# Kernel tuning notes

Hardware: AMD Instinct MI355X
Metric: run time of the kernel (lower is better)

Reference implementation:

```python
import jax, jax.numpy as jnp
import numpy as np

N = 50000   # nodes
E = 800000  # edges
H = 4       # heads
C = 64      # per-head channels (= hidden_channels, concat=False)
IN = 64     # in_channels
OUT = 32    # out_channels
EPS = 1e-5


def setup_inputs() -> dict:
    key = jax.random.key(0)
    ks = jax.random.split(key, 16)

    def lin(k, i, o):
        return (jax.random.normal(k, (i, o), jnp.float32) / np.sqrt(i)).astype(jnp.float32)

    inp = {}
    inp["x"] = jax.random.normal(ks[0], (N, IN), jnp.float32)
    inp["edge_index"] = jax.random.randint(ks[1], (2, E), 0, N, dtype=jnp.int32)
    # conv1 (in=IN)
    inp["Wq1"] = lin(ks[2], IN, H * C); inp["bq1"] = jnp.zeros((H * C,), jnp.float32)
    inp["Wk1"] = lin(ks[3], IN, H * C); inp["bk1"] = jnp.zeros((H * C,), jnp.float32)
    inp["Wv1"] = lin(ks[4], IN, H * C); inp["bv1"] = jnp.zeros((H * C,), jnp.float32)
    inp["Ws1"] = lin(ks[5], IN, C);     inp["bs1"] = jnp.zeros((C,), jnp.float32)
    # conv2 (in=head_out=C)
    inp["Wq2"] = lin(ks[6], C, H * C); inp["bq2"] = jnp.zeros((H * C,), jnp.float32)
    inp["Wk2"] = lin(ks[7], C, H * C); inp["bk2"] = jnp.zeros((H * C,), jnp.float32)
    inp["Wv2"] = lin(ks[8], C, H * C); inp["bv2"] = jnp.zeros((H * C,), jnp.float32)
    inp["Ws2"] = lin(ks[9], C, C);     inp["bs2"] = jnp.zeros((C,), jnp.float32)
    # shared LayerNorm over head_out=C, final Linear C->OUT
    inp["ln_g"] = jnp.ones((C,), jnp.float32)
    inp["ln_b"] = jnp.zeros((C,), jnp.float32)
    inp["Wf"] = lin(ks[10], C, OUT)
    inp["bf"] = jnp.zeros((OUT,), jnp.float32)
    return inp


def _layernorm(x, g, b):
    mu = jnp.mean(x, axis=-1, keepdims=True)
    var = jnp.mean(jnp.square(x - mu), axis=-1, keepdims=True)
    return (x - mu) * jax.lax.rsqrt(var + EPS) * g + b


def _transformer_conv(x, src, dst, Wq, bq, Wk, bk, Wv, bv, Ws, bs):
    # PyG TransformerConv, concat=False, beta=False, root_weight=True, eval dropout
    n = x.shape[0]
    q = (x @ Wq + bq).reshape(n, H, C)
    k = (x @ Wk + bk).reshape(n, H, C)
    v = (x @ Wv + bv).reshape(n, H, C)
    # per-edge attention logits [E, H]
    alpha = jnp.einsum('ehc,ehc->eh', q[dst], k[src]) / np.sqrt(C)
    # segment softmax over incoming edges of each dst node
    amax = jax.ops.segment_max(alpha, dst, num_segments=n)            # [N, H]
    ex = jnp.exp(alpha - amax[dst])                                   # [E, H]
    denom = jax.ops.segment_sum(ex, dst, num_segments=n)              # [N, H]
    attn = ex / (denom[dst] + 1e-16)                                  # [E, H]
    msg = attn[:, :, None] * v[src]                                   # [E, H, C]
    out = jax.ops.segment_sum(msg, dst, num_segments=n)               # [N, H, C]
    out = out.mean(axis=1)                                            # concat=False -> head mean
    return out + x @ Ws + bs                                          # skip connection


def reference(x, edge_index, Wq1, bq1, Wk1, bk1, Wv1, bv1, Ws1, bs1,
              Wq2, bq2, Wk2, bk2, Wv2, bv2, Ws2, bs2, ln_g, ln_b, Wf, bf):
    src, dst = edge_index[0], edge_index[1]
    h = _transformer_conv(x, src, dst, Wq1, bq1, Wk1, bk1, Wv1, bv1, Ws1, bs1)
    h = jax.nn.relu(_layernorm(h, ln_g, ln_b))  # dropout = identity (eval)
    h = _transformer_conv(h, src, dst, Wq2, bq2, Wk2, bk2, Wv2, bv2, Ws2, bs2)
    h = _layernorm(h, ln_g, ln_b)               # last layer: no relu/dropout
    return h @ Wf + bf
```

## Files before the change

kernel.cpp:

```cpp
#include <hip/hip_runtime.h>
#include <hip/hip_bf16.h>
#include <math.h>

typedef unsigned short u16;
typedef unsigned char u8;
typedef __attribute__((ext_vector_type(8))) short bf16x8;
typedef __attribute__((ext_vector_type(4))) float f32x4;
typedef __attribute__((ext_vector_type(2))) float f32x2;
typedef _Float16 f16;
typedef __attribute__((ext_vector_type(2))) _Float16 f16x2;

#if __has_builtin(__builtin_amdgcn_cvt_pk_f32_fp8) && __has_builtin(__builtin_amdgcn_cvt_pk_fp8_f32)
#define HAS_FP8 1
#else
#define HAS_FP8 0
#endif

__device__ __forceinline__ u16 f2bf(float f) {
    unsigned u = __float_as_uint(f);
    u += 0x7fffu + ((u >> 16) & 1u);
    return (u16)(u >> 16);
}
__device__ __forceinline__ u16 f2h(float f) {
    return __builtin_bit_cast(u16, (f16)f);
}
__device__ __forceinline__ f16x2 u2h(int u) {
    return __builtin_bit_cast(f16x2, u);
}

#if HAS_FP8
typedef uint2 kreg_t;
typedef uint2 vreg_t;
__device__ __forceinline__ float dotqk(kreg_t K, const float qf[8]) {
    f32x2 d0 = __builtin_amdgcn_cvt_pk_f32_fp8(K.x, false);
    f32x2 d1 = __builtin_amdgcn_cvt_pk_f32_fp8(K.x, true);
    f32x2 d2 = __builtin_amdgcn_cvt_pk_f32_fp8(K.y, false);
    f32x2 d3 = __builtin_amdgcn_cvt_pk_f32_fp8(K.y, true);
    float p = d0.x * qf[0];
    p = fmaf(d0.y, qf[1], p); p = fmaf(d1.x, qf[2], p); p = fmaf(d1.y, qf[3], p);
    p = fmaf(d2.x, qf[4], p); p = fmaf(d2.y, qf[5], p);
    p = fmaf(d3.x, qf[6], p); p = fmaf(d3.y, qf[7], p);
    return p;
}
__device__ __forceinline__ void dec8(vreg_t V, float w[8]) {
    f32x2 a0 = __builtin_amdgcn_cvt_pk_f32_fp8(V.x, false);
    f32x2 a1 = __builtin_amdgcn_cvt_pk_f32_fp8(V.x, true);
    f32x2 a2 = __builtin_amdgcn_cvt_pk_f32_fp8(V.y, false);
    f32x2 a3 = __builtin_amdgcn_cvt_pk_f32_fp8(V.y, true);
    w[0] = a0.x; w[1] = a0.y; w[2] = a1.x; w[3] = a1.y;
    w[4] = a2.x; w[5] = a2.y; w[6] = a3.x; w[7] = a3.y;
}
#else
typedef int4 kreg_t;
typedef int4 vreg_t;
__device__ __forceinline__ float dotqk(kreg_t K, const float qf[8]) {
    f16x2 t0 = u2h(K.x), t1 = u2h(K.y), t2 = u2h(K.z), t3 = u2h(K.w);
    float p = (float)t0.x * qf[0];
    p = fmaf((float)t0.y, qf[1], p); p = fmaf((float)t1.x, qf[2], p);
    p = fmaf((float)t1.y, qf[3], p); p = fmaf((float)t2.x, qf[4], p);
    p = fmaf((float)t2.y, qf[5], p); p = fmaf((float)t3.x, qf[6], p);
    p = fmaf((float)t3.y, qf[7], p);
    return p;
}
__device__ __forceinline__ void dec8(vreg_t V, float w[8]) {
    f16x2 t0 = u2h(V.x), t1 = u2h(V.y), t2 = u2h(V.z), t3 = u2h(V.w);
    w[0] = (float)t0.x; w[1] = (float)t0.y;
    w[2] = (float)t1.x; w[3] = (float)t1.y;
    w[4] = (float)t2.x; w[5] = (float)t2.y;
    w[6] = (float)t3.x; w[7] = (float)t3.y;
}
#endif

__device__ __forceinline__ void conv_w_one(
    int idx,
    const float* __restrict__ Wq, const float* __restrict__ Wk,
    const float* __restrict__ Wv, const float* __restrict__ Ws,
    const float* __restrict__ bq, const float* __restrict__ bk,
    const float* __restrict__ bv, const float* __restrict__ bs,
    u16* __restrict__ wt, float* __restrict__ ba)
{
    int col = idx >> 6, k = idx & 63;
    float w;
    if      (col < 256) w = Wq[k * 256 + col] * 0.125f;
    else if (col < 512) w = Wk[k * 256 + (col - 256)];
    else if (col < 768) w = Wv[k * 256 + (col - 512)];
    else                w = Ws[k * 64  + (col - 768)];
    wt[col * 64 + k] = f2bf(w);
    if (k == 0)
        ba[col] = (col < 256) ? bq[col] * 0.125f : (col < 512) ? bk[col - 256]
                 : (col < 768) ? bv[col - 512] : bs[col - 768];
}

__global__ __launch_bounds__(256) void prep_misc(
    const float* __restrict__ Wq1, const float* __restrict__ Wk1,
    const float* __restrict__ Wv1, const float* __restrict__ Ws1,
    const float* __restrict__ bq1, const float* __restrict__ bk1,
    const float* __restrict__ bv1, const float* __restrict__ bs1,
    const float* __restrict__ Wq2, const float* __restrict__ Wk2,
    const float* __restrict__ Wv2, const float* __restrict__ Ws2,
    const float* __restrict__ bq2, const float* __restrict__ bk2,
    const float* __restrict__ bv2, const float* __restrict__ bs2,
    u16* __restrict__ wt1, float* __restrict__ ba1,
    u16* __restrict__ wt2, float* __restrict__ ba2,
    int* __restrict__ deg, int n)
{
    int b = blockIdx.x, t = threadIdx.x;
    if (b < 208) {
        conv_w_one(b * 256 + t, Wq1, Wk1, Wv1, Ws1, bq1, bk1, bv1, bs1, wt1, ba1);
    } else if (b < 416) {
        conv_w_one((b - 208) * 256 + t, Wq2, Wk2, Wv2, Ws2, bq2, bk2, bv2, bs2, wt2, ba2);
    } else {
        int i = (b - 416) * 256 + t;
        if (i < n) deg[i] = 0;
    }
}

__global__ __launch_bounds__(256) void scanA(
    const int* __restrict__ deg, int* __restrict__ bsum, int n)
{
    int i = blockIdx.x * 256 + threadIdx.x;
    int v = (i < n) ? deg[i] : 0;
    #pragma unroll
    for (int o = 32; o; o >>= 1) v += __shfl_xor(v, o);
    __shared__ int wsum[4];
    if ((threadIdx.x & 63) == 0) wsum[threadIdx.x >> 6] = v;
    __syncthreads();
    if (threadIdx.x == 0)
        bsum[blockIdx.x] = wsum[0] + wsum[1] + wsum[2] + wsum[3];
}

__global__ __launch_bounds__(256) void scanB(
    const int* __restrict__ bsum, int* __restrict__ bpre, int nb)
{
    int t = threadIdx.x;
    int v = (t < nb) ? bsum[t] : 0;
    int lane = t & 63, wv = t >> 6;
    int sv = v;
    #pragma unroll
    for (int o = 1; o < 64; o <<= 1) {
        int u = __shfl_up(sv, o);
        if (lane >= o) sv += u;
    }
    __shared__ int wsum[4];
    if (lane == 63) wsum[wv] = sv;
    __syncthreads();
    int add = 0;
    for (int k = 0; k < wv; ++k) add += wsum[k];
    if (t < nb) bpre[t] = sv + add - v;
}

__global__ __launch_bounds__(256) void scanC(
    const int* __restrict__ deg, const int* __restrict__ bpre,
    int* __restrict__ off, int* __restrict__ cursor, int n, int E)
{
    int i = blockIdx.x * 256 + threadIdx.x;
    int v = (i < n) ? deg[i] : 0;
    int lane = threadIdx.x & 63, wv = threadIdx.x >> 6;
    int sv = v;
    #pragma unroll
    for (int o = 1; o < 64; o <<= 1) {
        int u = __shfl_up(sv, o);
        if (lane >= o) sv += u;
    }
    __shared__ int wsum[4];
    if (lane == 63) wsum[wv] = sv;
    __syncthreads();
    int add = bpre[blockIdx.x];
    for (int k = 0; k < wv; ++k) add += wsum[k];
    int excl = add + sv - v;
    if (i < n) {
        off[i] = excl; cursor[i] = excl;
        if (i == n - 1) off[n] = E;
    }
}

__global__ __launch_bounds__(256) void fill_kernel(
    const int* __restrict__ src, const int* __restrict__ dst,
    int* __restrict__ cursor, int* __restrict__ csr_src, int E)
{
    int e = blockIdx.x * 256 + threadIdx.x;
    if (e >= E) return;
    int slot = atomicAdd(&cursor[dst[e]], 1);
    csr_src[slot] = src[e];
}

template <int FP32IN>
__device__ __forceinline__ void gemm_body(
    int blk, const void* __restrict__ Xv, const u16* __restrict__ wt,
    const float* __restrict__ ba,
    u16* __restrict__ qb, u8* __restrict__ kb8, u8* __restrict__ vb8,
    u16* __restrict__ skip, int n)
{
    const int w = threadIdx.x >> 6, lane = threadIdx.x & 63;
    const int r = lane & 15, g = lane >> 4;
    const int node0 = blk * 16;

    int nr = node0 + r; if (nr >= n) nr = n - 1;
    bf16x8 b0, b1;
    if (FP32IN) {
        const float* xr = (const float*)Xv + (size_t)nr * 64 + g * 8;
        float t0[8], t1[8];
        *(float4*)(t0)     = ((const float4*)xr)[0];
        *(float4*)(t0 + 4) = ((const float4*)xr)[1];
        *(float4*)(t1)     = ((const float4*)(xr + 32))[0];
        *(float4*)(t1 + 4) = ((const float4*)(xr + 32))[1];
        #pragma unroll
        for (int j = 0; j < 8; ++j) {
            b0[j] = (short)f2bf(t0[j]);
            b1[j] = (short)f2bf(t1[j]);
        }
    } else {
        const u16* xr = (const u16*)Xv + (size_t)nr * 64 + g * 8;
        b0 = *(const bf16x8*)xr;
        b1 = *(const bf16x8*)(xr + 32);
    }

    const int colbase = w * 208;
    const int node = node0 + r;

    const u16* wr0 = wt + (size_t)(colbase + r) * 64 + g * 8;
    bf16x8 a0 = *(const bf16x8*)wr0;
    bf16x8 a1 = *(const bf16x8*)(wr0 + 32);

    for (int ct = 0; ct < 13; ++ct) {
        int ctn = (ct + 1 < 13) ? ct + 1 : 12;
        const u16* wrn = wt + (size_t)(colbase + ctn * 16 + r) * 64 + g * 8;
        bf16x8 an0 = *(const bf16x8*)wrn;
        bf16x8 an1 = *(const bf16x8*)(wrn + 32);

        f32x4 acc = {0.f, 0.f, 0.f, 0.f};
        acc = __builtin_amdgcn_mfma_f32_16x16x32_bf16(a0, b0, acc, 0, 0, 0);
        acc = __builtin_amdgcn_mfma_f32_16x16x32_bf16(a1, b1, acc, 0, 0, 0);
        int col0 = colbase + ct * 16 + g * 4;
        float4 bias = *(const float4*)(ba + col0);
        if (node < n) {
            float v0 = acc[0] + bias.x, v1 = acc[1] + bias.y;
            float v2 = acc[2] + bias.z, v3 = acc[3] + bias.w;
            if (col0 < 256) {
                ushort4 o;
                o.x = f2h(v0); o.y = f2h(v1); o.z = f2h(v2); o.w = f2h(v3);
                *(ushort4*)(qb + (size_t)node * 256 + col0) = o;
            } else if (col0 < 512) {
                int c = col0 - 256;
#if HAS_FP8
                unsigned pk = __builtin_amdgcn_cvt_pk_fp8_f32(v0, v1, 0u, false);
                pk = __builtin_amdgcn_cvt_pk_fp8_f32(v2, v3, pk, true);
                *(unsigned*)(kb8 + (size_t)node * 256 + c) = pk;
#else
                ushort4 o;
                o.x = f2h(v0); o.y = f2h(v1); o.z = f2h(v2); o.w = f2h(v3);
                *(ushort4*)((u16*)kb8 + (size_t)node * 256 + c) = o;
#endif
            } else if (col0 < 768) {
                int c = col0 - 512;
#if HAS_FP8
                unsigned pk = __builtin_amdgcn_cvt_pk_fp8_f32(v0, v1, 0u, false);
                pk = __builtin_amdgcn_cvt_pk_fp8_f32(v2, v3, pk, true);
                *(unsigned*)(vb8 + (size_t)node * 256 + c) = pk;
#else
                ushort4 o;
                o.x = f2h(v0); o.y = f2h(v1); o.z = f2h(v2); o.w = f2h(v3);
                *(ushort4*)((u16*)vb8 + (size_t)node * 256 + c) = o;
#endif
            } else {
                ushort4 o;
                o.x = f2h(v0); o.y = f2h(v1); o.z = f2h(v2); o.w = f2h(v3);
                *(ushort4*)(skip + (size_t)node * 64 + (col0 - 768)) = o;
            }
        }
        a0 = an0; a1 = an1;
    }
}

__global__ __launch_bounds__(256) void gemm1_hist(
    const float* __restrict__ x, const u16* __restrict__ wt,
    const float* __restrict__ ba,
    u16* __restrict__ qb, u8* __restrict__ kb8, u8* __restrict__ vb8,
    u16* __restrict__ skip, int n,
    const int* __restrict__ dst, int* __restrict__ deg, int E, int gb)
{
    int b = blockIdx.x;
    if (b < gb) {
        gemm_body<1>(b, x, wt, ba, qb, kb8, vb8, skip, n);
    } else {
        int e = (b - gb) * 256 + threadIdx.x;
        if (e < E) atomicAdd(&deg[dst[e]], 1);
    }
}

__global__ __launch_bounds__(256) void gemm_qkvs2(
    const u16* __restrict__ xbf, const u16* __restrict__ wt,
    const float* __restrict__ ba,
    u16* __restrict__ qb, u8* __restrict__ kb8, u8* __restrict__ vb8,
    u16* __restrict__ skip, int n)
{
    gemm_body<0>(blockIdx.x, xbf, wt, ba, qb, kb8, vb8, skip, n);
}

template <int RELU, int BF16OUT, int FINAL>
__global__ __launch_bounds__(256) void fused_attn(
    const u16* __restrict__ qb, const u8* __restrict__ kb8,
    const u8* __restrict__ vb8, const u16* __restrict__ skip,
    const int* __restrict__ off, const int* __restrict__ csr,
    const float* __restrict__ lng, const float* __restrict__ lnb,
    u16* __restrict__ out_bf,
    const float* __restrict__ Wf, const float* __restrict__ bfv,
    float* __restrict__ outF, int n)
{
    const int lane = threadIdx.x & 63;
    const int half = lane >> 5;
    const int hl   = lane & 31;
    const int c8   = lane & 7;
    const int wv   = threadIdx.x >> 6;
    const int node = blockIdx.x * 4 + wv;
    const bool nvalid = node < n;
    const int nodeC = nvalid ? node : n - 1;

    const int4 qw = *(const int4*)(qb + (size_t)nodeC * 256 + hl * 8);
    float qf[8];
    {
        f16x2 t0 = u2h(qw.x), t1 = u2h(qw.y), t2 = u2h(qw.z), t3 = u2h(qw.w);
        qf[0] = (float)t0.x; qf[1] = (float)t0.y;
        qf[2] = (float)t1.x; qf[3] = (float)t1.y;
        qf[4] = (float)t2.x; qf[5] = (float)t2.y;
        qf[6] = (float)t3.x; qf[7] = (float)t3.y;
    }

    const int s0 = off[nodeC], s1 = off[nodeC + 1];
    const int deg = nvalid ? (s1 - s0) : 0;
    const int imax = (deg + 1) >> 1;

    float m = -1e30f, l = 0.f;
    float a[8] = {0.f, 0.f, 0.f, 0.f, 0.f, 0.f, 0.f, 0.f};

    if (imax > 0) {
#if HAS_FP8
        const u8* kbase = kb8 + hl * 8;
        const u8* vbase = vb8 + hl * 8;
#else
        const u16* kbase = (const u16*)kb8 + hl * 8;
        const u16* vbase = (const u16*)vb8 + hl * 8;
#endif
        #define LOADKV(I, K, V) { \
            int _ix = min(s0 + 2 * (I) + half, s1 - 1); \
            int _s = csr[_ix]; \
            K = *(const kreg_t*)(kbase + (size_t)_s * 256); \
            V = *(const vreg_t*)(vbase + (size_t)_s * 256); }

        kreg_t k0, k1, k2;
        vreg_t v0, v1, v2;
        LOADKV(0, k0, v0);
        LOADKV(1, k1, v1);
        LOADKV(2, k2, v2);

        #pragma unroll 3
        for (int i = 0; i < imax; ++i) {
            kreg_t kn; vreg_t vn;
            LOADKV(i + 3, kn, vn);

            float p = dotqk(k0, qf);
            p += __shfl_xor(p, 1);
            p += __shfl_xor(p, 2);
            p += __shfl_xor(p, 4);
            p = (2 * i + half < deg) ? p : -2e30f;

            float w[8];
            dec8(v0, w);
            if (__all(p - m <= 8.f)) {
                float e = __expf(p - m);
                l += e;
                #pragma unroll
                for (int j = 0; j < 8; ++j) a[j] = fmaf(e, w[j], a[j]);
            } else {
                float nm = fmaxf(m, p);
                float c = __expf(m - nm);
                float e = __expf(p - nm);
                m = nm;
                l = l * c + e;
                #pragma unroll
                for (int j = 0; j < 8; ++j) a[j] = fmaf(e, w[j], a[j] * c);
            }

            k0 = k1; v0 = v1; k1 = k2; v1 = v2; k2 = kn; v2 = vn;
        }
        #undef LOADKV
    }

    {
        float mo = __shfl_xor(m, 32);
        float lo_ = __shfl_xor(l, 32);
        float nm = fmaxf(m, mo);
        float c  = __expf(m - nm);
        float co = __expf(mo - nm);
        l = l * c + lo_ * co;
        #pragma unroll
        for (int j = 0; j < 8; ++j) {
            float ao = __shfl_xor(a[j], 32);
            a[j] = a[j] * c + ao * co;
        }
    }

    const float inv = 0.25f / (l + 1e-16f);
    #pragma unroll
    for (int j = 0; j < 8; ++j) {
        a[j] *= inv;
        a[j] += __shfl_xor(a[j], 8);
        a[j] += __shfl_xor(a[j], 16);
    }

    const int4 skw = *(const int4*)(skip + (size_t)nodeC * 64 + c8 * 8);
    f16x2 s0_ = u2h(skw.x), s1_ = u2h(skw.y), s2_ = u2h(skw.z), s3_ = u2h(skw.w);
    float o[8];
    o[0] = a[0] + (float)s0_.x; o[1] = a[1] + (float)s0_.y;
    o[2] = a[2] + (float)s1_.x; o[3] = a[3] + (float)s1_.y;
    o[4] = a[4] + (float)s2_.x; o[5] = a[5] + (float)s2_.y;
    o[6] = a[6] + (float)s3_.x; o[7] = a[7] + (float)s3_.y;

    float s = o[0] + o[1] + o[2] + o[3] + o[4] + o[5] + o[6] + o[7];
    s += __shfl_xor(s, 1); s += __shfl_xor(s, 2); s += __shfl_xor(s, 4);
    const float mu = s * (1.f / 64.f);
    float vs = 0.f;
    #pragma unroll
    for (int j = 0; j < 8; ++j) { o[j] -= mu; vs = fmaf(o[j], o[j], vs); }
    vs += __shfl_xor(vs, 1); vs += __shfl_xor(vs, 2); vs += __shfl_xor(vs, 4);
    const float rs = rsqrtf(vs * (1.f / 64.f) + 1e-5f);

    const float4* gp = (const float4*)(lng + c8 * 8);
    const float4* bp = (const float4*)(lnb + c8 * 8);
    float4 g0 = gp[0], g1 = gp[1], b0 = bp[0], b1 = bp[1];
    float y[8];
    y[0] = o[0] * rs * g0.x + b0.x; y[1] = o[1] * rs * g0.y + b0.y;
    y[2] = o[2] * rs * g0.z + b0.z; y[3] = o[3] * rs * g0.w + b0.w;
    y[4] = o[4] * rs * g1.x + b1.x; y[5] = o[5] * rs * g1.y + b1.y;
    y[6] = o[6] * rs * g1.z + b1.z; y[7] = o[7] * rs * g1.w + b1.w;
    if (RELU) {
        #pragma unroll
        for (int j = 0; j < 8; ++j) y[j] = fmaxf(y[j], 0.f);
    }

    if (FINAL) {
        __shared__ float yl[4][64];
        if (lane < 8) {
            #pragma unroll
            for (int j = 0; j < 8; ++j) yl[wv][c8 * 8 + j] = y[j];
        }
        __syncthreads();
        int t = threadIdx.x;
        if (t < 128) {
            int nd = t >> 5, oc = t & 31;
            int gn = blockIdx.x * 4 + nd;
            if (gn < n) {
                float acc = bfv[oc];
                #pragma unroll
                for (int c = 0; c < 64; ++c)
                    acc = fmaf(yl[nd][c], Wf[c * 32 + oc], acc);
                outF[(size_t)gn * 32 + oc] = acc;
            }
        }
    } else if (lane < 8 && nvalid) {
        if (BF16OUT) {
            bf16x8 ob;
            #pragma unroll
            for (int j = 0; j < 8; ++j) ob[j] = (short)f2bf(y[j]);
            *(bf16x8*)(out_bf + (size_t)node * 64 + c8 * 8) = ob;
        }
    }
}

extern "C" void kernel_launch(void* const* d_in, const int* in_sizes, int n_in,
                              void* d_out, int out_size, void* d_ws, size_t ws_size,
                              hipStream_t stream)
{
    const float* x   = (const float*)d_in[0];
    const int*   ei  = (const int*)d_in[1];
    const float* Wq1 = (const float*)d_in[2];  const float* bq1 = (const float*)d_in[3];
    const float* Wk1 = (const float*)d_in[4];  const float* bk1 = (const float*)d_in[5];
    const float* Wv1 = (const float*)d_in[6];  const float* bv1 = (const float*)d_in[7];
    const float* Ws1 = (const float*)d_in[8];  const float* bs1 = (const float*)d_in[9];
    const float* Wq2 = (const float*)d_in[10]; const float* bq2 = (const float*)d_in[11];
    const float* Wk2 = (const float*)d_in[12]; const float* bk2 = (const float*)d_in[13];
    const float* Wv2 = (const float*)d_in[14]; const float* bv2 = (const float*)d_in[15];
    const float* Ws2 = (const float*)d_in[16]; const float* bs2 = (const float*)d_in[17];
    const float* lng = (const float*)d_in[18]; const float* lnb = (const float*)d_in[19];
    const float* Wf  = (const float*)d_in[20]; const float* bf  = (const float*)d_in[21];

    const int N = in_sizes[0] / 64;
    const int E = in_sizes[1] / 2;
    const int* src  = ei;
    const int* dstp = ei + E;

    char* p = (char*)d_ws;
    u16* qb   = (u16*)p; p += (size_t)N * 256 * 2;
    u8*  kb8  = (u8*)p;  p += (size_t)N * 256 * 2;
    u8*  vb8  = (u8*)p;  p += (size_t)N * 256 * 2;
    u16* xbf  = (u16*)p; p += (size_t)N * 64 * 2;
    u16* wt1  = (u16*)p; p += 832 * 64 * 2;
    u16* wt2  = (u16*)p; p += 832 * 64 * 2;
    float* ba1  = (float*)p; p += 832 * 4;
    float* ba2  = (float*)p; p += 832 * 4;
    u16* skip = (u16*)p; p += (size_t)N * 64 * 2;
    int* deg    = (int*)p; p += (size_t)N * 4;
    int* off    = (int*)p; p += ((size_t)N + 1) * 4;
    int* cursor = (int*)p; p += (size_t)N * 4;
    int* csr    = (int*)p; p += (size_t)E * 4;
    int* bsum   = (int*)p; p += 1024;
    int* bpre   = (int*)p; p += 1024;

    const int e_blocks    = (E + 255) / 256;
    const int n_blocks    = (N + 255) / 256;
    const int prep_blocks = 416 + n_blocks;
    const int gb          = (N + 15) / 16;
    const int attn_blocks = (N + 3) / 4;

    prep_misc<<<prep_blocks, 256, 0, stream>>>(
        Wq1, Wk1, Wv1, Ws1, bq1, bk1, bv1, bs1,
        Wq2, Wk2, Wv2, Ws2, bq2, bk2, bv2, bs2,
        wt1, ba1, wt2, ba2, deg, N);

    gemm1_hist<<<gb + e_blocks, 256, 0, stream>>>(
        x, wt1, ba1, qb, kb8, vb8, skip, N, dstp, deg, E, gb);

    scanA<<<n_blocks, 256, 0, stream>>>(deg, bsum, N);
    scanB<<<1, 256, 0, stream>>>(bsum, bpre, n_blocks);
    scanC<<<n_blocks, 256, 0, stream>>>(deg, bpre, off, cursor, N, E);
    fill_kernel<<<e_blocks, 256, 0, stream>>>(src, dstp, cursor, csr, E);

    fused_attn<1, 1, 0><<<attn_blocks, 256, 0, stream>>>(
        qb, kb8, vb8, skip, off, csr, lng, lnb, xbf, nullptr, nullptr, nullptr, N);

    gemm_qkvs2<<<gb, 256, 0, stream>>>(xbf, wt2, ba2, qb, kb8, vb8, skip, N);

    fused_attn<0, 0, 1><<<attn_blocks, 256, 0, stream>>>(
        qb, kb8, vb8, skip, off, csr, lng, lnb, nullptr, Wf, bf, (float*)d_out, N);
}
```

Before: 368.2 us.

## Interleave K and V per node into one buffer and double GEMM rows per block

K and V projections are now stored interleaved in a single buffer: for each head-lane slice, 8 K bytes sit next to 8 V bytes, so the attention gather for one edge does a single 16-byte load instead of two 8-byte loads from separate arrays. This is meant to halve the number of scattered gather transactions per edge and improve cache-line use in the memory-bound attention kernels. The GEMM kernel also handles 32 nodes per block (two MFMA groups) so each weight tile load is reused twice, halving the GEMM grid. The non-FP8 fallback path is duplicated with its own layout.

```diff
diff --git a/kernel.cpp b/kernel.cpp
--- a/kernel.cpp
+++ b/kernel.cpp
@@ -29,31 +29,27 @@
 }
 
 #if HAS_FP8
-typedef uint2 kreg_t;
-typedef uint2 vreg_t;
-__device__ __forceinline__ float dotqk(kreg_t K, const float qf[8]) {
-    f32x2 d0 = __builtin_amdgcn_cvt_pk_f32_fp8(K.x, false);
-    f32x2 d1 = __builtin_amdgcn_cvt_pk_f32_fp8(K.x, true);
-    f32x2 d2 = __builtin_amdgcn_cvt_pk_f32_fp8(K.y, false);
-    f32x2 d3 = __builtin_amdgcn_cvt_pk_f32_fp8(K.y, true);
+__device__ __forceinline__ float dotqk2(unsigned lo, unsigned hi, const float qf[8]) {
+    f32x2 d0 = __builtin_amdgcn_cvt_pk_f32_fp8(lo, false);
+    f32x2 d1 = __builtin_amdgcn_cvt_pk_f32_fp8(lo, true);
+    f32x2 d2 = __builtin_amdgcn_cvt_pk_f32_fp8(hi, false);
+    f32x2 d3 = __builtin_amdgcn_cvt_pk_f32_fp8(hi, true);
     float p = d0.x * qf[0];
     p = fmaf(d0.y, qf[1], p); p = fmaf(d1.x, qf[2], p); p = fmaf(d1.y, qf[3], p);
     p = fmaf(d2.x, qf[4], p); p = fmaf(d2.y, qf[5], p);
     p = fmaf(d3.x, qf[6], p); p = fmaf(d3.y, qf[7], p);
     return p;
 }
-__device__ __forceinline__ void dec8(vreg_t V, float w[8]) {
-    f32x2 a0 = __builtin_amdgcn_cvt_pk_f32_fp8(V.x, false);
-    f32x2 a1 = __builtin_amdgcn_cvt_pk_f32_fp8(V.x, true);
-    f32x2 a2 = __builtin_amdgcn_cvt_pk_f32_fp8(V.y, false);
-    f32x2 a3 = __builtin_amdgcn_cvt_pk_f32_fp8(V.y, true);
+__device__ __forceinline__ void dec8v(unsigned lo, unsigned hi, float w[8]) {
+    f32x2 a0 = __builtin_amdgcn_cvt_pk_f32_fp8(lo, false);
+    f32x2 a1 = __builtin_amdgcn_cvt_pk_f32_fp8(lo, true);
+    f32x2 a2 = __builtin_amdgcn_cvt_pk_f32_fp8(hi, false);
+    f32x2 a3 = __builtin_amdgcn_cvt_pk_f32_fp8(hi, true);
     w[0] = a0.x; w[1] = a0.y; w[2] = a1.x; w[3] = a1.y;
     w[4] = a2.x; w[5] = a2.y; w[6] = a3.x; w[7] = a3.y;
 }
 #else
-typedef int4 kreg_t;
-typedef int4 vreg_t;
-__device__ __forceinline__ float dotqk(kreg_t K, const float qf[8]) {
+__device__ __forceinline__ float dotqk_h(int4 K, const float qf[8]) {
     f16x2 t0 = u2h(K.x), t1 = u2h(K.y), t2 = u2h(K.z), t3 = u2h(K.w);
     float p = (float)t0.x * qf[0];
     p = fmaf((float)t0.y, qf[1], p); p = fmaf((float)t1.x, qf[2], p);
@@ -62,7 +58,7 @@
     p = fmaf((float)t3.y, qf[7], p);
     return p;
 }
-__device__ __forceinline__ void dec8(vreg_t V, float w[8]) {
+__device__ __forceinline__ void dec8_h(int4 V, float w[8]) {
     f16x2 t0 = u2h(V.x), t1 = u2h(V.y), t2 = u2h(V.z), t3 = u2h(V.w);
     w[0] = (float)t0.x; w[1] = (float)t0.y;
     w[2] = (float)t1.x; w[3] = (float)t1.y;
@@ -188,35 +184,36 @@
 __device__ __forceinline__ void gemm_body(
     int blk, const void* __restrict__ Xv, const u16* __restrict__ wt,
     const float* __restrict__ ba,
-    u16* __restrict__ qb, u8* __restrict__ kb8, u8* __restrict__ vb8,
-    u16* __restrict__ skip, int n)
+    u16* __restrict__ qb, u8* __restrict__ kvb, u16* __restrict__ skip, int n)
 {
     const int w = threadIdx.x >> 6, lane = threadIdx.x & 63;
     const int r = lane & 15, g = lane >> 4;
-    const int node0 = blk * 16;
-
-    int nr = node0 + r; if (nr >= n) nr = n - 1;
-    bf16x8 b0, b1;
-    if (FP32IN) {
-        const float* xr = (const float*)Xv + (size_t)nr * 64 + g * 8;
-        float t0[8], t1[8];
-        *(float4*)(t0)     = ((const float4*)xr)[0];
-        *(float4*)(t0 + 4) = ((const float4*)xr)[1];
-        *(float4*)(t1)     = ((const float4*)(xr + 32))[0];
-        *(float4*)(t1 + 4) = ((const float4*)(xr + 32))[1];
-        #pragma unroll
-        for (int j = 0; j < 8; ++j) {
-            b0[j] = (short)f2bf(t0[j]);
-            b1[j] = (short)f2bf(t1[j]);
-        }
-    } else {
-        const u16* xr = (const u16*)Xv + (size_t)nr * 64 + g * 8;
-        b0 = *(const bf16x8*)xr;
-        b1 = *(const bf16x8*)(xr + 32);
+    const int node0 = blk * 32;
+
+    bf16x8 bx0[2], bx1[2];
+    #pragma unroll
+    for (int grp = 0; grp < 2; ++grp) {
+        int nr = node0 + grp * 16 + r; if (nr >= n) nr = n - 1;
+        if (FP32IN) {
+            const float* xr = (const float*)Xv + (size_t)nr * 64 + g * 8;
+            float t0[8], t1[8];
+            *(float4*)(t0)     = ((const float4*)xr)[0];
+            *(float4*)(t0 + 4) = ((const float4*)xr)[1];
+            *(float4*)(t1)     = ((const float4*)(xr + 32))[0];
+            *(float4*)(t1 + 4) = ((const float4*)(xr + 32))[1];
+            #pragma unroll
+            for (int j = 0; j < 8; ++j) {
+                bx0[grp][j] = (short)f2bf(t0[j]);
+                bx1[grp][j] = (short)f2bf(t1[j]);
+            }
+        } else {
+            const u16* xr = (const u16*)Xv + (size_t)nr * 64 + g * 8;
+            bx0[grp] = *(const bf16x8*)xr;
+            bx1[grp] = *(const bf16x8*)(xr + 32);
+        }
     }
 
     const int colbase = w * 208;
-    const int node = node0 + r;
 
     const u16* wr0 = wt + (size_t)(colbase + r) * 64 + g * 8;
     bf16x8 a0 = *(const bf16x8*)wr0;
@@ -228,44 +225,41 @@
         bf16x8 an0 = *(const bf16x8*)wrn;
         bf16x8 an1 = *(const bf16x8*)(wrn + 32);
 
-        f32x4 acc = {0.f, 0.f, 0.f, 0.f};
-        acc = __builtin_amdgcn_mfma_f32_16x16x32_bf16(a0, b0, acc, 0, 0, 0);
-        acc = __builtin_amdgcn_mfma_f32_16x16x32_bf16(a1, b1, acc, 0, 0, 0);
         int col0 = colbase + ct * 16 + g * 4;
         float4 bias = *(const float4*)(ba + col0);
-        if (node < n) {
-            float v0 = acc[0] + bias.x, v1 = acc[1] + bias.y;
-            float v2 = acc[2] + bias.z, v3 = acc[3] + bias.w;
-            if (col0 < 256) {
-                ushort4 o;
-                o.x = f2h(v0); o.y = f2h(v1); o.z = f2h(v2); o.w = f2h(v3);
-                *(ushort4*)(qb + (size_t)node * 256 + col0) = o;
-            } else if (col0 < 512) {
-                int c = col0 - 256;
+
+        #pragma unroll
+        for (int grp = 0; grp < 2; ++grp) {
+            f32x4 acc = {0.f, 0.f, 0.f, 0.f};
+            acc = __builtin_amdgcn_mfma_f32_16x16x32_bf16(a0, bx0[grp], acc, 0, 0, 0);
+            acc = __builtin_amdgcn_mfma_f32_16x16x32_bf16(a1, bx1[grp], acc, 0, 0, 0);
+            int node = node0 + grp * 16 + r;
+            if (node < n) {
+                float v0 = acc[0] + bias.x, v1 = acc[1] + bias.y;
+                float v2 = acc[2] + bias.z, v3 = acc[3] + bias.w;
+                if (col0 < 256) {
+                    ushort4 o;
+                    o.x = f2h(v0); o.y = f2h(v1); o.z = f2h(v2); o.w = f2h(v3);
+                    *(ushort4*)(qb + (size_t)node * 256 + col0) = o;
+                } else if (col0 < 768) {
+                    const bool isK = col0 < 512;
+                    int c = col0 - (isK ? 256 : 512);
 #if HAS_FP8
-                unsigned pk = __builtin_amdgcn_cvt_pk_fp8_f32(v0, v1, 0u, false);
-                pk = __builtin_amdgcn_cvt_pk_fp8_f32(v2, v3, pk, true);
-                *(unsigned*)(kb8 + (size_t)node * 256 + c) = pk;
+                    unsigned pk = __builtin_amdgcn_cvt_pk_fp8_f32(v0, v1, 0u, false);
+                    pk = __builtin_amdgcn_cvt_pk_fp8_f32(v2, v3, pk, true);
+                    *(unsigned*)(kvb + (size_t)node * 512 + ((c >> 3) << 4)
+                                 + (c & 7) + (isK ? 0 : 8)) = pk;
 #else
-                ushort4 o;
-                o.x = f2h(v0); o.y = f2h(v1); o.z = f2h(v2); o.w = f2h(v3);
-                *(ushort4*)((u16*)kb8 + (size_t)node * 256 + c) = o;
+                    ushort4 o;
+                    o.x = f2h(v0); o.y = f2h(v1); o.z = f2h(v2); o.w = f2h(v3);
+                    *(ushort4*)(kvb + (size_t)node * 1024 + ((c >> 3) << 5)
+                                + ((c & 7) << 1) + (isK ? 0 : 16)) = o;
 #endif
-            } else if (col0 < 768) {
-                int c = col0 - 512;
-#if HAS_FP8
-                unsigned pk = __builtin_amdgcn_cvt_pk_fp8_f32(v0, v1, 0u, false);
-                pk = __builtin_amdgcn_cvt_pk_fp8_f32(v2, v3, pk, true);
-                *(unsigned*)(vb8 + (size_t)node * 256 + c) = pk;
-#else
-                ushort4 o;
-                o.x = f2h(v0); o.y = f2h(v1); o.z = f2h(v2); o.w = f2h(v3);
-                *(ushort4*)((u16*)vb8 + (size_t)node * 256 + c) = o;
-#endif
-            } else {
-                ushort4 o;
-                o.x = f2h(v0); o.y = f2h(v1); o.z = f2h(v2); o.w = f2h(v3);
-                *(ushort4*)(skip + (size_t)node * 64 + (col0 - 768)) = o;
+                } else {
+                    ushort4 o;
+                    o.x = f2h(v0); o.y = f2h(v1); o.z = f2h(v2); o.w = f2h(v3);
+                    *(ushort4*)(skip + (size_t)node * 64 + (col0 - 768)) = o;
+                }
             }
         }
         a0 = an0; a1 = an1;
@@ -275,13 +269,12 @@
 __global__ __launch_bounds__(256) void gemm1_hist(
     const float* __restrict__ x, const u16* __restrict__ wt,
     const float* __restrict__ ba,
-    u16* __restrict__ qb, u8* __restrict__ kb8, u8* __restrict__ vb8,
-    u16* __restrict__ skip, int n,
+    u16* __restrict__ qb, u8* __restrict__ kvb, u16* __restrict__ skip, int n,
     const int* __restrict__ dst, int* __restrict__ deg, int E, int gb)
 {
     int b = blockIdx.x;
     if (b < gb) {
-        gemm_body<1>(b, x, wt, ba, qb, kb8, vb8, skip, n);
+        gemm_body<1>(b, x, wt, ba, qb, kvb, skip, n);
     } else {
         int e = (b - gb) * 256 + threadIdx.x;
         if (e < E) atomicAdd(&deg[dst[e]], 1);
@@ -291,16 +284,15 @@
 __global__ __launch_bounds__(256) void gemm_qkvs2(
     const u16* __restrict__ xbf, const u16* __restrict__ wt,
     const float* __restrict__ ba,
-    u16* __restrict__ qb, u8* __restrict__ kb8, u8* __restrict__ vb8,
-    u16* __restrict__ skip, int n)
-{
-    gemm_body<0>(blockIdx.x, xbf, wt, ba, qb, kb8, vb8, skip, n);
+    u16* __restrict__ qb, u8* __restrict__ kvb, u16* __restrict__ skip, int n)
+{
+    gemm_body<0>(blockIdx.x, xbf, wt, ba, qb, kvb, skip, n);
 }
 
 template <int RELU, int BF16OUT, int FINAL>
 __global__ __launch_bounds__(256) void fused_attn(
-    const u16* __restrict__ qb, const u8* __restrict__ kb8,
-    const u8* __restrict__ vb8, const u16* __restrict__ skip,
+    const u16* __restrict__ qb, const u8* __restrict__ kvb,
+    const u16* __restrict__ skip,
     const int* __restrict__ off, const int* __restrict__ csr,
     const float* __restrict__ lng, const float* __restrict__ lnb,
     u16* __restrict__ out_bf,
@@ -335,37 +327,30 @@
 
     if (imax > 0) {
 #if HAS_FP8
-        const u8* kbase = kb8 + hl * 8;
-        const u8* vbase = vb8 + hl * 8;
-#else
-        const u16* kbase = (const u16*)kb8 + hl * 8;
-        const u16* vbase = (const u16*)vb8 + hl * 8;
-#endif
-        #define LOADKV(I, K, V) { \
+        const u8* kvbase = kvb + hl * 16;
+        #define LOADKV(I, KV) { \
             int _ix = min(s0 + 2 * (I) + half, s1 - 1); \
             int _s = csr[_ix]; \
-            K = *(const kreg_t*)(kbase + (size_t)_s * 256); \
-            V = *(const vreg_t*)(vbase + (size_t)_s * 256); }
-
-        kreg_t k0, k1, k2;
-        vreg_t v0, v1, v2;
-        LOADKV(0, k0, v0);
-        LOADKV(1, k1, v1);
-        LOADKV(2, k2, v2);
+            KV = *(const uint4*)(kvbase + (size_t)_s * 512); }
+
+        uint4 kv0, kv1, kv2;
+        LOADKV(0, kv0);
+        LOADKV(1, kv1);
+        LOADKV(2, kv2);
 
         #pragma unroll 3
         for (int i = 0; i < imax; ++i) {
-            kreg_t kn; vreg_t vn;
-            LOADKV(i + 3, kn, vn);
-
-            float p = dotqk(k0, qf);
+            uint4 kvn;
+            LOADKV(i + 3, kvn);
+
+            float p = dotqk2(kv0.x, kv0.y, qf);
             p += __shfl_xor(p, 1);
             p += __shfl_xor(p, 2);
             p += __shfl_xor(p, 4);
             p = (2 * i + half < deg) ? p : -2e30f;
 
             float w[8];
-            dec8(v0, w);
+            dec8v(kv0.z, kv0.w, w);
             if (__all(p - m <= 8.f)) {
                 float e = __expf(p - m);
                 l += e;
@@ -381,9 +366,54 @@
                 for (int j = 0; j < 8; ++j) a[j] = fmaf(e, w[j], a[j] * c);
             }
 
+            kv0 = kv1; kv1 = kv2; kv2 = kvn;
+        }
+        #undef LOADKV
+#else
+        const u8* kvbase = kvb + hl * 32;
+        #define LOADKV(I, K, V) { \
+            int _ix = min(s0 + 2 * (I) + half, s1 - 1); \
+            int _s = csr[_ix]; \
+            K = *(const int4*)(kvbase + (size_t)_s * 1024); \
+            V = *(const int4*)(kvbase + (size_t)_s * 1024 + 16); }
+
+        int4 k0, k1, k2, v0, v1, v2;
+        LOADKV(0, k0, v0);
+        LOADKV(1, k1, v1);
+        LOADKV(2, k2, v2);
+
+        #pragma unroll 3
+        for (int i = 0; i < imax; ++i) {
+            int4 kn, vn;
+            LOADKV(i + 3, kn, vn);
+
+            float p = dotqk_h(k0, qf);
+            p += __shfl_xor(p, 1);
+            p += __shfl_xor(p, 2);
+            p += __shfl_xor(p, 4);
+            p = (2 * i + half < deg) ? p : -2e30f;
+
+            float w[8];
+            dec8_h(v0, w);
+            if (__all(p - m <= 8.f)) {
+                float e = __expf(p - m);
+                l += e;
+                #pragma unroll
+                for (int j = 0; j < 8; ++j) a[j] = fmaf(e, w[j], a[j]);
+            } else {
+                float nm = fmaxf(m, p);
+                float c = __expf(m - nm);
+                float e = __expf(p - nm);
+                m = nm;
+                l = l * c + e;
+                #pragma unroll
+                for (int j = 0; j < 8; ++j) a[j] = fmaf(e, w[j], a[j] * c);
+            }
+
             k0 = k1; v0 = v1; k1 = k2; v1 = v2; k2 = kn; v2 = vn;
         }
         #undef LOADKV
+#endif
     }
 
     {
@@ -491,8 +521,7 @@
 
     char* p = (char*)d_ws;
     u16* qb   = (u16*)p; p += (size_t)N * 256 * 2;
-    u8*  kb8  = (u8*)p;  p += (size_t)N * 256 * 2;
-    u8*  vb8  = (u8*)p;  p += (size_t)N * 256 * 2;
+    u8*  kvb  = (u8*)p;  p += (size_t)N * 1024;
     u16* xbf  = (u16*)p; p += (size_t)N * 64 * 2;
     u16* wt1  = (u16*)p; p += 832 * 64 * 2;
     u16* wt2  = (u16*)p; p += 832 * 64 * 2;
@@ -509,7 +538,7 @@
     const int e_blocks    = (E + 255) / 256;
     const int n_blocks    = (N + 255) / 256;
     const int prep_blocks = 416 + n_blocks;
-    const int gb          = (N + 15) / 16;
+    const int gb          = (N + 31) / 32;
     const int attn_blocks = (N + 3) / 4;
 
     prep_misc<<<prep_blocks, 256, 0, stream>>>(
@@ -518,7 +547,7 @@
         wt1, ba1, wt2, ba2, deg, N);
 
     gemm1_hist<<<gb + e_blocks, 256, 0, stream>>>(
-        x, wt1, ba1, qb, kb8, vb8, skip, N, dstp, deg, E, gb);
+        x, wt1, ba1, qb, kvb, skip, N, dstp, deg, E, gb);
 
     scanA<<<n_blocks, 256, 0, stream>>>(deg, bsum, N);
     scanB<<<1, 256, 0, stream>>>(bsum, bpre, n_blocks);
@@ -526,10 +555,10 @@
     fill_kernel<<<e_blocks, 256, 0, stream>>>(src, dstp, cursor, csr, E);
 
     fused_attn<1, 1, 0><<<attn_blocks, 256, 0, stream>>>(
-        qb, kb8, vb8, skip, off, csr, lng, lnb, xbf, nullptr, nullptr, nullptr, N);
-
-    gemm_qkvs2<<<gb, 256, 0, stream>>>(xbf, wt2, ba2, qb, kb8, vb8, skip, N);
+        qb, kvb, skip, off, csr, lng, lnb, xbf, nullptr, nullptr, nullptr, N);
+
+    gemm_qkvs2<<<gb, 256, 0, stream>>>(xbf, wt2, ba2, qb, kvb, skip, N);
 
     fused_attn<0, 0, 1><<<attn_blocks, 256, 0, stream>>>(
-        qb, kb8, vb8, skip, off, csr, lng, lnb, nullptr, Wf, bf, (float*)d_out, N);
-}
+        qb, kvb, skip, off, csr, lng, lnb, nullptr, Wf, bf, (float*)d_out, N);
+}
```

After: 335.3 us. -8.9%, faster.
